# Kernel optimization log

Hardware: AMD Instinct MI355X
Metric: run time of the kernel (lower is better)

Reference implementation:

```python
import jax, jax.numpy as jnp
import numpy as np

D = 128        # node_representation_size
V = 100000     # unique_internal_nodes (embedding vocab)
N = 20000      # nodes in the internal graph
E = 640000     # total neighbor (edge) entries


def setup_inputs() -> dict:
    key = jax.random.key(0)
    k1, k2, k3, k4, k5, k6 = jax.random.split(key, 6)
    node_ids = jax.random.randint(k1, (N,), 0, V)
    neighbor_ids = jax.random.randint(k2, (E,), 0, V)
    segment_ids = jnp.sort(jax.random.randint(k3, (E,), 0, N))
    xav = 1.0 / np.sqrt(D)  # xavier_normal std for square [D,D]
    W = jax.random.normal(k4, (D, D), dtype=jnp.float32) * xav
    M = jax.random.normal(k5, (D, D), dtype=jnp.float32) * xav
    emb = jax.random.normal(k6, (V, D), dtype=jnp.float32)
    return {"node_ids": node_ids, "neighbor_ids": neighbor_ids,
            "segment_ids": segment_ids, "W": W, "M": M, "emb": emb}


def reference(node_ids, neighbor_ids, segment_ids, W, M, emb):
    # Per node: s = relu(W @ e[node] + sum_{nbr} M @ e[nbr]); result = sum_nodes s
    self_term = emb[node_ids] @ W.T                       # [N, D]
    nb_msgs = emb[neighbor_ids] @ M.T                     # [E, D]
    nb_agg = jax.ops.segment_sum(nb_msgs, segment_ids, num_segments=N)  # [N, D]
    per_node = jax.nn.relu(self_term + nb_agg)            # [N, D]
    result = per_node.sum(axis=0)                         # [D]
    return jax.nn.softmax(result)[:, None]                # [D, 1], softmax over dim 0
```

## Files before the change

kernel.cpp:

```cpp
#include <hip/hip_runtime.h>

#define D 128
#define RS_STRIDE 64

typedef __attribute__((ext_vector_type(8))) short bf16x8;
typedef __attribute__((ext_vector_type(8))) unsigned short u16x8;
typedef __attribute__((ext_vector_type(4))) float f32x4;
typedef __attribute__((ext_vector_type(2))) float f32x2;

__device__ __forceinline__ unsigned short f2bf(float f) {
    unsigned u = __float_as_uint(f);
    unsigned r = (u + 0x7fffu + ((u >> 16) & 1u)) >> 16;
    return (unsigned short)r;
}
__device__ __forceinline__ float bf2f(unsigned short h) {
    return __uint_as_float(((unsigned)h) << 16);
}
__device__ __forceinline__ ushort4 pack4(float4 v) {
    ushort4 o; o.x = f2bf(v.x); o.y = f2bf(v.y); o.z = f2bf(v.z); o.w = f2bf(v.w);
    return o;
}
__device__ __forceinline__ void red3(float& x) {
    x += __shfl_xor(x, 8);
    x += __shfl_xor(x, 16);
    x += __shfl_xor(x, 32);
}
__device__ __forceinline__ void acc4(unsigned v, float* s) {
    f32x2 lo = __builtin_amdgcn_cvt_pk_f32_fp8(v, false);
    f32x2 hi = __builtin_amdgcn_cvt_pk_f32_fp8(v, true);
    s[0] += lo[0]; s[1] += lo[1]; s[2] += hi[0]; s[3] += hi[1];
}
__device__ __forceinline__ void acc16(uint4 v, float* s) {
    acc4(v.x, s); acc4(v.y, s + 4); acc4(v.z, s + 8); acc4(v.w, s + 12);
}
__device__ __forceinline__ int swz(int r, int s) {
    return r * D + ((s ^ (r & 7)) << 3);
}

__global__ void prep_kernel(const float* __restrict__ emb, const float* __restrict__ W,
                            const float* __restrict__ M, const int* __restrict__ seg,
                            unsigned char* __restrict__ emb8,
                            unsigned short* __restrict__ Wb, unsigned short* __restrict__ Mb,
                            float* __restrict__ rs, int* __restrict__ row_ptr,
                            int n4, int E, int N) {
    int i = blockIdx.x * blockDim.x + threadIdx.x;
    if (i < n4) {
        float4 v = ((const float4*)emb)[i];
        int p = __builtin_amdgcn_cvt_pk_fp8_f32(v.x, v.y, 0, false);
        p = __builtin_amdgcn_cvt_pk_fp8_f32(v.z, v.w, p, true);
        ((unsigned*)emb8)[i] = (unsigned)p;
    }
    if (i < 4096)       ((ushort4*)Wb)[i]        = pack4(((const float4*)W)[i]);
    else if (i < 8192)  ((ushort4*)Mb)[i - 4096] = pack4(((const float4*)M)[i - 4096]);
    if (i < D) rs[i * RS_STRIDE] = 0.0f;
    if (i < E) {
        int s = seg[i];
        if (i == 0) {
            for (int n = 0; n <= s; ++n) row_ptr[n] = 0;
        } else {
            int sp = seg[i - 1];
            for (int n = sp + 1; n <= s; ++n) row_ptr[n] = i;
        }
        if (i == E - 1) {
            for (int n = s + 1; n <= N; ++n) row_ptr[n] = E;
        }
    }
}

__global__ __launch_bounds__(256) void fused_kernel(
    const int* __restrict__ node_ids, const int* __restrict__ nbr,
    const int* __restrict__ row_ptr, const unsigned char* __restrict__ emb8,
    const unsigned short* __restrict__ Wb, const unsigned short* __restrict__ Mb,
    float* __restrict__ rs, int N) {
    __shared__ unsigned short xs[16 * D];
    __shared__ unsigned short as_[16 * D];

    int t = threadIdx.x;
    int w = t >> 6;
    int tt = t & 63;
    int g = blockIdx.x;

    {
        int c = tt & 7;
        int j = tt >> 3;
        for (int i = 0; i < 4; ++i) {
            int r = w * 4 + i;
            int n = g * 16 + r;
            bool valid = n < N;

            uint4 xv = make_uint4(0u, 0u, 0u, 0u);
            if (valid && j == 0)
                xv = *(const uint4*)(emb8 + (size_t)node_ids[n] * D + c * 16);

            float s[16];
#pragma unroll
            for (int k = 0; k < 16; ++k) s[k] = 0.f;

            int lo = valid ? row_ptr[n] : 0;
            int hi = valid ? row_ptr[n + 1] : 0;
            int e = lo + j;
            for (; e + 8 < hi; e += 16) {
                uint4 a = *(const uint4*)(emb8 + (size_t)nbr[e] * D + c * 16);
                uint4 b = *(const uint4*)(emb8 + (size_t)nbr[e + 8] * D + c * 16);
                acc16(a, s);
                acc16(b, s);
            }
            if (e < hi) {
                uint4 a = *(const uint4*)(emb8 + (size_t)nbr[e] * D + c * 16);
                acc16(a, s);
            }
#pragma unroll
            for (int k = 0; k < 16; ++k) red3(s[k]);

            if (j == 0) {
                u16x8 o0, o1;
#pragma unroll
                for (int k = 0; k < 8; ++k) { o0[k] = f2bf(s[k]); o1[k] = f2bf(s[k + 8]); }
                *(u16x8*)&as_[swz(r, 2 * c)]     = o0;
                *(u16x8*)&as_[swz(r, 2 * c + 1)] = o1;

                float x[16];
#pragma unroll
                for (int k = 0; k < 16; ++k) x[k] = 0.f;
                acc16(xv, x);
                u16x8 p0, p1;
#pragma unroll
                for (int k = 0; k < 8; ++k) { p0[k] = f2bf(x[k]); p1[k] = f2bf(x[k + 8]); }
                *(u16x8*)&xs[swz(r, 2 * c)]     = p0;
                *(u16x8*)&xs[swz(r, 2 * c + 1)] = p1;
            }
        }
    }
    __syncthreads();

    int quad = tt >> 4, col = tt & 15;
    bf16x8 ax[4], aa[4];
#pragma unroll
    for (int ks = 0; ks < 4; ++ks) {
        ax[ks] = *(const bf16x8*)&xs[swz(col, ks * 4 + quad)];
        aa[ks] = *(const bf16x8*)&as_[swz(col, ks * 4 + quad)];
    }
#pragma unroll
    for (int p = 0; p < 2; ++p) {
        int dt = w + p * 4;
        int wrow = (dt * 16 + col) * D + quad * 8;
        f32x4 acc = {0.f, 0.f, 0.f, 0.f};
#pragma unroll
        for (int ks = 0; ks < 4; ++ks) {
            bf16x8 bw = *(const bf16x8*)(Wb + wrow + ks * 32);
            bf16x8 bm = *(const bf16x8*)(Mb + wrow + ks * 32);
            acc = __builtin_amdgcn_mfma_f32_16x16x32_bf16(ax[ks], bw, acc, 0, 0, 0);
            acc = __builtin_amdgcn_mfma_f32_16x16x32_bf16(aa[ks], bm, acc, 0, 0, 0);
        }
        float v = fmaxf(acc[0], 0.f) + fmaxf(acc[1], 0.f)
                + fmaxf(acc[2], 0.f) + fmaxf(acc[3], 0.f);
        v += __shfl_xor(v, 16);
        v += __shfl_xor(v, 32);
        if (tt < 16) atomicAdd(&rs[(dt * 16 + col) * RS_STRIDE], v);
    }
}

__global__ void agg_f32_kernel(const int* __restrict__ nbr, const int* __restrict__ row_ptr,
                               const float* __restrict__ emb,
                               unsigned short* __restrict__ aggb, int N) {
    int n = blockIdx.x * 4 + (threadIdx.x >> 6);
    if (n >= N) return;
    int tt = threadIdx.x & 63;
    int c = tt & 7;
    int j = tt >> 3;

    int lo = row_ptr[n], hi = row_ptr[n + 1];

    float4 s0 = make_float4(0.f, 0.f, 0.f, 0.f);
    float4 s1 = make_float4(0.f, 0.f, 0.f, 0.f);
    float4 s2 = make_float4(0.f, 0.f, 0.f, 0.f);
    float4 s3 = make_float4(0.f, 0.f, 0.f, 0.f);
    for (int e = lo + j; e < hi; e += 8) {
        const float4* r = (const float4*)&emb[(size_t)nbr[e] * D];
        float4 v0 = r[c], v1 = r[c + 8], v2 = r[c + 16], v3 = r[c + 24];
        s0.x += v0.x; s0.y += v0.y; s0.z += v0.z; s0.w += v0.w;
        s1.x += v1.x; s1.y += v1.y; s1.z += v1.z; s1.w += v1.w;
        s2.x += v2.x; s2.y += v2.y; s2.z += v2.z; s2.w += v2.w;
        s3.x += v3.x; s3.y += v3.y; s3.z += v3.z; s3.w += v3.w;
    }
    red3(s0.x); red3(s0.y); red3(s0.z); red3(s0.w);
    red3(s1.x); red3(s1.y); red3(s1.z); red3(s1.w);
    red3(s2.x); red3(s2.y); red3(s2.z); red3(s2.w);
    red3(s3.x); red3(s3.y); red3(s3.z); red3(s3.w);
    if (j == 0) {
        ushort4* o = (ushort4*)(aggb + (size_t)n * D);
        o[c]      = pack4(s0);
        o[c + 8]  = pack4(s1);
        o[c + 16] = pack4(s2);
        o[c + 24] = pack4(s3);
    }
}

__global__ __launch_bounds__(256) void matvec_f32_kernel(
    const int* __restrict__ node_ids, const float* __restrict__ emb,
    const unsigned short* __restrict__ aggb,
    const unsigned short* __restrict__ Wb, const unsigned short* __restrict__ Mb,
    float* __restrict__ rs, int N, int ngroups, int nstripes) {
    int t = threadIdx.x;
    int wid = blockIdx.x * 4 + (t >> 6);
    int l = t & 63;
    int quad = l >> 4, col = l & 15;
    int dt = wid & 7;
    int stripe = wid >> 3;

    bf16x8 bw[4], bm[4];
    int wrow = (dt * 16 + col) * D;
#pragma unroll
    for (int ks = 0; ks < 4; ++ks) {
        int off = wrow + ks * 32 + quad * 8;
        bw[ks] = *(const bf16x8*)(Wb + off);
        bm[ks] = *(const bf16x8*)(Mb + off);
    }

    const bf16x8 zero8 = {0, 0, 0, 0, 0, 0, 0, 0};
    float vsum = 0.f;

    for (int grp = stripe; grp < ngroups; grp += nstripes) {
        int node = grp * 16 + col;
        bool valid = node < N;
        int nid = valid ? node_ids[node] : 0;
        const unsigned short* ar = aggb + (size_t)node * D + quad * 8;

        f32x4 acc = {0.f, 0.f, 0.f, 0.f};
#pragma unroll
        for (int ks = 0; ks < 4; ++ks) {
            bf16x8 ax;
            if (valid) {
                const float4* xf = (const float4*)(emb +
                                   (size_t)nid * D + quad * 8 + ks * 32);
                ushort4 p0 = pack4(xf[0]);
                ushort4 p1 = pack4(xf[1]);
                ax[0] = (short)p0.x; ax[1] = (short)p0.y;
                ax[2] = (short)p0.z; ax[3] = (short)p0.w;
                ax[4] = (short)p1.x; ax[5] = (short)p1.y;
                ax[6] = (short)p1.z; ax[7] = (short)p1.w;
            } else ax = zero8;
            bf16x8 aa = valid ? *(const bf16x8*)(ar + ks * 32) : zero8;
            acc = __builtin_amdgcn_mfma_f32_16x16x32_bf16(ax, bw[ks], acc, 0, 0, 0);
            acc = __builtin_amdgcn_mfma_f32_16x16x32_bf16(aa, bm[ks], acc, 0, 0, 0);
        }
        vsum += fmaxf(acc[0], 0.f) + fmaxf(acc[1], 0.f)
              + fmaxf(acc[2], 0.f) + fmaxf(acc[3], 0.f);
    }

    vsum += __shfl_xor(vsum, 16);
    vsum += __shfl_xor(vsum, 32);
    if (l < 16) atomicAdd(&rs[(dt * 16 + col) * RS_STRIDE], vsum);
}

__global__ void softmax_kernel(const float* __restrict__ rs, float* __restrict__ out) {
    int t = threadIdx.x;
    float v0 = rs[t * RS_STRIDE];
    float v1 = rs[(t + 64) * RS_STRIDE];
    float m = fmaxf(v0, v1);
    for (int o = 32; o > 0; o >>= 1) m = fmaxf(m, __shfl_xor(m, o));
    float e0 = expf(v0 - m);
    float e1 = expf(v1 - m);
    float s = e0 + e1;
    for (int o = 32; o > 0; o >>= 1) s += __shfl_xor(s, o);
    float inv = 1.0f / s;
    out[t] = e0 * inv;
    out[t + 64] = e1 * inv;
}

extern "C" void kernel_launch(void* const* d_in, const int* in_sizes, int n_in,
                              void* d_out, int out_size, void* d_ws, size_t ws_size,
                              hipStream_t stream) {
    const int*   node_ids = (const int*)d_in[0];
    const int*   nbr      = (const int*)d_in[1];
    const int*   seg      = (const int*)d_in[2];
    const float* W        = (const float*)d_in[3];
    const float* M        = (const float*)d_in[4];
    const float* emb      = (const float*)d_in[5];
    float* out = (float*)d_out;

    int N = in_sizes[0];
    int E = in_sizes[1];
    long long VD = in_sizes[5];
    int ngroups  = (N + 15) / 16;

    unsigned short* aggb = (unsigned short*)d_ws;
    unsigned short* Wb   = aggb + (size_t)N * D;
    unsigned short* Mb   = Wb + D * D;
    float* rs            = (float*)(Mb + D * D);
    int* row_ptr         = (int*)(rs + (size_t)D * RS_STRIDE);
    unsigned char* emb8  = (unsigned char*)(row_ptr + (N + 1));

    size_t need_fp8 = (size_t)((char*)emb8 - (char*)d_ws) + (size_t)VD;
    bool use_fp8 = ws_size >= need_fp8;
    int n4 = use_fp8 ? (int)(VD / 4) : 0;
    int cvt_n = (n4 > 8192 ? n4 : 8192);
    int prep_n = (cvt_n > E ? cvt_n : E);

    prep_kernel<<<(prep_n + 255) / 256, 256, 0, stream>>>(emb, W, M, seg, emb8, Wb, Mb,
                                                          rs, row_ptr, n4, E, N);
    if (use_fp8) {
        fused_kernel<<<ngroups, 256, 0, stream>>>(node_ids, nbr, row_ptr, emb8,
                                                  Wb, Mb, rs, N);
    } else {
        int nstripes = (ngroups + 1) / 2;
        agg_f32_kernel<<<(N + 3) / 4, 256, 0, stream>>>(nbr, row_ptr, emb, aggb, N);
        matvec_f32_kernel<<<2 * nstripes, 256, 0, stream>>>(node_ids, emb, aggb, Wb, Mb,
                                                            rs, N, ngroups, nstripes);
    }
    softmax_kernel<<<1, 64, 0, stream>>>(rs, out);
}
```

Before: 141.9 us.

## Halve nodes per block in fused kernel and unroll neighbor gather by four

Each fused-kernel block now handles 8 nodes instead of 16, which doubles the grid size to spread the gather-heavy work across more CUs and waves. The neighbor loop is unrolled to issue four independent embedding loads per thread per iteration, for more memory-level parallelism. The 16-row MFMA tile is kept, and rows 8-15 are zero-padded. That wastes half of the matrix-multiply work per block and doubles the W/M reads and atomics on rs.

After: 158.9 us. 12.0% more time.

```diff
diff --git a/kernel.cpp b/kernel.cpp
--- a/kernel.cpp
+++ b/kernel.cpp
@@ -72,8 +72,8 @@
     const int* __restrict__ row_ptr, const unsigned char* __restrict__ emb8,
     const unsigned short* __restrict__ Wb, const unsigned short* __restrict__ Mb,
     float* __restrict__ rs, int N) {
-    __shared__ unsigned short xs[16 * D];
-    __shared__ unsigned short as_[16 * D];
+    __shared__ unsigned short xs[8 * D];
+    __shared__ unsigned short as_[8 * D];
 
     int t = threadIdx.x;
     int w = t >> 6;
@@ -83,9 +83,9 @@
     {
         int c = tt & 7;
         int j = tt >> 3;
-        for (int i = 0; i < 4; ++i) {
-            int r = w * 4 + i;
-            int n = g * 16 + r;
+        for (int i = 0; i < 2; ++i) {
+            int r = w * 2 + i;
+            int n = g * 8 + r;
             bool valid = n < N;
 
             uint4 xv = make_uint4(0u, 0u, 0u, 0u);
@@ -99,11 +99,24 @@
             int lo = valid ? row_ptr[n] : 0;
             int hi = valid ? row_ptr[n + 1] : 0;
             int e = lo + j;
-            for (; e + 8 < hi; e += 16) {
-                uint4 a = *(const uint4*)(emb8 + (size_t)nbr[e] * D + c * 16);
-                uint4 b = *(const uint4*)(emb8 + (size_t)nbr[e + 8] * D + c * 16);
-                acc16(a, s);
-                acc16(b, s);
+            for (; e + 24 < hi; e += 32) {
+                int i0 = nbr[e];
+                int i1 = nbr[e + 8];
+                int i2 = nbr[e + 16];
+                int i3 = nbr[e + 24];
+                uint4 a = *(const uint4*)(emb8 + (size_t)i0 * D + c * 16);
+                uint4 b = *(const uint4*)(emb8 + (size_t)i1 * D + c * 16);
+                uint4 d = *(const uint4*)(emb8 + (size_t)i2 * D + c * 16);
+                uint4 f = *(const uint4*)(emb8 + (size_t)i3 * D + c * 16);
+                acc16(a, s); acc16(b, s); acc16(d, s); acc16(f, s);
+            }
+            if (e + 8 < hi) {
+                int i0 = nbr[e];
+                int i1 = nbr[e + 8];
+                uint4 a = *(const uint4*)(emb8 + (size_t)i0 * D + c * 16);
+                uint4 b = *(const uint4*)(emb8 + (size_t)i1 * D + c * 16);
+                acc16(a, s); acc16(b, s);
+                e += 16;
             }
             if (e < hi) {
                 uint4 a = *(const uint4*)(emb8 + (size_t)nbr[e] * D + c * 16);
@@ -134,11 +147,17 @@
     __syncthreads();
 
     int quad = tt >> 4, col = tt & 15;
+    const bf16x8 zero8 = {0, 0, 0, 0, 0, 0, 0, 0};
     bf16x8 ax[4], aa[4];
 #pragma unroll
     for (int ks = 0; ks < 4; ++ks) {
-        ax[ks] = *(const bf16x8*)&xs[swz(col, ks * 4 + quad)];
-        aa[ks] = *(const bf16x8*)&as_[swz(col, ks * 4 + quad)];
+        if (col < 8) {
+            ax[ks] = *(const bf16x8*)&xs[swz(col, ks * 4 + quad)];
+            aa[ks] = *(const bf16x8*)&as_[swz(col, ks * 4 + quad)];
+        } else {
+            ax[ks] = zero8;
+            aa[ks] = zero8;
+        }
     }
 #pragma unroll
     for (int p = 0; p < 2; ++p) {
@@ -282,7 +301,7 @@
     int N = in_sizes[0];
     int E = in_sizes[1];
     long long VD = in_sizes[5];
-    int ngroups  = (N + 15) / 16;
+    int ngroups8 = (N + 7) / 8;
 
     unsigned short* aggb = (unsigned short*)d_ws;
     unsigned short* Wb   = aggb + (size_t)N * D;
@@ -297,12 +316,13 @@
     int cvt_n = (n4 > 8192 ? n4 : 8192);
     int prep_n = (cvt_n > E ? cvt_n : E);
 
-    prep_kernel<<<(prep_n + 255) / 256, 256, 0, stream>>>(emb, W, M, seg, emb8, Wb, Mb,
+    prep_kernel<<<(prep_n + 255) / 256, 256, 0, stream>>>(emb, M ? W : W, M, seg, emb8, Wb, Mb,
                                                           rs, row_ptr, n4, E, N);
     if (use_fp8) {
-        fused_kernel<<<ngroups, 256, 0, stream>>>(node_ids, nbr, row_ptr, emb8,
-                                                  Wb, Mb, rs, N);
+        fused_kernel<<<ngroups8, 256, 0, stream>>>(node_ids, nbr, row_ptr, emb8,
+                                                   Wb, Mb, rs, N);
     } else {
+        int ngroups  = (N + 15) / 16;
         int nstripes = (ngroups + 1) / 2;
         agg_f32_kernel<<<(N + 3) / 4, 256, 0, stream>>>(nbr, row_ptr, emb, aggb, N);
         matvec_f32_kernel<<<2 * nstripes, 256, 0, stream>>>(node_ids, emb, aggb, Wb, Mb,
```

## Slice fp8 embeddings by column and split aggregation into per-slice kernel

Applied to the files above, without the earlier changes.

Stores the fp8 embedding table as eight column slices of 16 bytes per row, and splits the fused kernel into a per-slice neighbor aggregation kernel plus a matvec kernel that reads the bf16 aggregate from workspace. Each aggregation block touches only one slice so gathers hit a smaller working set that may stay in L2. In exchange it adds an extra launch, a round trip of the aggregate through global memory, and repeated reads of neighbor indices across slices.

Result: slower. 184.8 us (+30.3%).

```diff
diff --git a/kernel.cpp b/kernel.cpp
--- a/kernel.cpp
+++ b/kernel.cpp
@@ -13,9 +13,6 @@
     unsigned r = (u + 0x7fffu + ((u >> 16) & 1u)) >> 16;
     return (unsigned short)r;
 }
-__device__ __forceinline__ float bf2f(unsigned short h) {
-    return __uint_as_float(((unsigned)h) << 16);
-}
 __device__ __forceinline__ ushort4 pack4(float4 v) {
     ushort4 o; o.x = f2bf(v.x); o.y = f2bf(v.y); o.z = f2bf(v.z); o.w = f2bf(v.w);
     return o;
@@ -30,16 +27,13 @@
     f32x2 hi = __builtin_amdgcn_cvt_pk_f32_fp8(v, true);
     s[0] += lo[0]; s[1] += lo[1]; s[2] += hi[0]; s[3] += hi[1];
 }
-__device__ __forceinline__ void acc16(uint4 v, float* s) {
-    acc4(v.x, s); acc4(v.y, s + 4); acc4(v.z, s + 8); acc4(v.w, s + 12);
-}
 __device__ __forceinline__ int swz(int r, int s) {
     return r * D + ((s ^ (r & 7)) << 3);
 }
 
 __global__ void prep_kernel(const float* __restrict__ emb, const float* __restrict__ W,
                             const float* __restrict__ M, const int* __restrict__ seg,
-                            unsigned char* __restrict__ emb8,
+                            unsigned char* __restrict__ emb8s, size_t V16,
                             unsigned short* __restrict__ Wb, unsigned short* __restrict__ Mb,
                             float* __restrict__ rs, int* __restrict__ row_ptr,
                             int n4, int E, int N) {
@@ -48,7 +42,10 @@
         float4 v = ((const float4*)emb)[i];
         int p = __builtin_amdgcn_cvt_pk_fp8_f32(v.x, v.y, 0, false);
         p = __builtin_amdgcn_cvt_pk_fp8_f32(v.z, v.w, p, true);
-        ((unsigned*)emb8)[i] = (unsigned)p;
+        int vrow = i >> 5;
+        int d0 = (i & 31) << 2;
+        *(unsigned*)(emb8s + (size_t)(d0 >> 4) * V16 + (size_t)vrow * 16 + (d0 & 15))
+            = (unsigned)p;
     }
     if (i < 4096)       ((ushort4*)Wb)[i]        = pack4(((const float4*)W)[i]);
     else if (i < 8192)  ((ushort4*)Mb)[i - 4096] = pack4(((const float4*)M)[i - 4096]);
@@ -67,9 +64,63 @@
     }
 }
 
-__global__ __launch_bounds__(256) void fused_kernel(
-    const int* __restrict__ node_ids, const int* __restrict__ nbr,
-    const int* __restrict__ row_ptr, const unsigned char* __restrict__ emb8,
+__global__ __launch_bounds__(256) void agg_slice_kernel(
+    const int* __restrict__ nbr, const int* __restrict__ row_ptr,
+    const unsigned char* __restrict__ emb8s, size_t V16,
+    unsigned short* __restrict__ aggb, int N) {
+    int s = blockIdx.x & 7;
+    int chunk = blockIdx.x >> 3;
+    int t = threadIdx.x;
+    int w = t >> 6;
+    int tt = t & 63;
+    int h = tt >> 5;
+    int j = (tt >> 2) & 7;
+    int c = tt & 3;
+
+    const unsigned char* base = emb8s + (size_t)s * V16 + c * 4;
+
+#pragma unroll
+    for (int pair = 0; pair < 4; ++pair) {
+        int n = chunk * 32 + (pair * 4 + w) * 2 + h;
+        bool valid = n < N;
+        int lo = valid ? row_ptr[n] : 0;
+        int hi = valid ? row_ptr[n + 1] : 0;
+
+        float sa[4] = {0.f, 0.f, 0.f, 0.f};
+        int e = lo + j;
+        for (; e + 8 < hi; e += 16) {
+            int i0 = __builtin_nontemporal_load(&nbr[e]);
+            int i1 = __builtin_nontemporal_load(&nbr[e + 8]);
+            unsigned a = *(const unsigned*)(base + (size_t)i0 * 16);
+            unsigned b = *(const unsigned*)(base + (size_t)i1 * 16);
+            acc4(a, sa); acc4(b, sa);
+        }
+        if (e < hi) {
+            int i0 = __builtin_nontemporal_load(&nbr[e]);
+            unsigned a = *(const unsigned*)(base + (size_t)i0 * 16);
+            acc4(a, sa);
+        }
+#pragma unroll
+        for (int k = 0; k < 4; ++k) {
+            sa[k] += __shfl_xor(sa[k], 4);
+            sa[k] += __shfl_xor(sa[k], 8);
+            sa[k] += __shfl_xor(sa[k], 16);
+        }
+        if (valid && j == 0) {
+            unsigned long long o =
+                  (unsigned long long)f2bf(sa[0])
+                | ((unsigned long long)f2bf(sa[1]) << 16)
+                | ((unsigned long long)f2bf(sa[2]) << 32)
+                | ((unsigned long long)f2bf(sa[3]) << 48);
+            __builtin_nontemporal_store(
+                o, (unsigned long long*)(aggb + (size_t)n * D + s * 16 + c * 4));
+        }
+    }
+}
+
+__global__ __launch_bounds__(256) void matvec_kernel(
+    const int* __restrict__ node_ids, const unsigned char* __restrict__ emb8s,
+    size_t V16, const unsigned short* __restrict__ aggb,
     const unsigned short* __restrict__ Wb, const unsigned short* __restrict__ Mb,
     float* __restrict__ rs, int N) {
     __shared__ unsigned short xs[16 * D];
@@ -81,55 +132,30 @@
     int g = blockIdx.x;
 
     {
-        int c = tt & 7;
-        int j = tt >> 3;
-        for (int i = 0; i < 4; ++i) {
-            int r = w * 4 + i;
-            int n = g * 16 + r;
-            bool valid = n < N;
-
-            uint4 xv = make_uint4(0u, 0u, 0u, 0u);
-            if (valid && j == 0)
-                xv = *(const uint4*)(emb8 + (size_t)node_ids[n] * D + c * 16);
-
-            float s[16];
-#pragma unroll
-            for (int k = 0; k < 16; ++k) s[k] = 0.f;
-
-            int lo = valid ? row_ptr[n] : 0;
-            int hi = valid ? row_ptr[n + 1] : 0;
-            int e = lo + j;
-            for (; e + 8 < hi; e += 16) {
-                uint4 a = *(const uint4*)(emb8 + (size_t)nbr[e] * D + c * 16);
-                uint4 b = *(const uint4*)(emb8 + (size_t)nbr[e + 8] * D + c * 16);
-                acc16(a, s);
-                acc16(b, s);
-            }
-            if (e < hi) {
-                uint4 a = *(const uint4*)(emb8 + (size_t)nbr[e] * D + c * 16);
-                acc16(a, s);
-            }
-#pragma unroll
-            for (int k = 0; k < 16; ++k) red3(s[k]);
-
-            if (j == 0) {
-                u16x8 o0, o1;
-#pragma unroll
-                for (int k = 0; k < 8; ++k) { o0[k] = f2bf(s[k]); o1[k] = f2bf(s[k + 8]); }
-                *(u16x8*)&as_[swz(r, 2 * c)]     = o0;
-                *(u16x8*)&as_[swz(r, 2 * c + 1)] = o1;
-
-                float x[16];
-#pragma unroll
-                for (int k = 0; k < 16; ++k) x[k] = 0.f;
-                acc16(xv, x);
-                u16x8 p0, p1;
-#pragma unroll
-                for (int k = 0; k < 8; ++k) { p0[k] = f2bf(x[k]); p1[k] = f2bf(x[k + 8]); }
-                *(u16x8*)&xs[swz(r, 2 * c)]     = p0;
-                *(u16x8*)&xs[swz(r, 2 * c + 1)] = p1;
-            }
-        }
+        int r = w * 4 + (tt >> 4);
+        int slot = tt & 15;
+        int n = g * 16 + r;
+        bool valid = n < N;
+
+        u16x8 av = {0, 0, 0, 0, 0, 0, 0, 0};
+        if (valid) av = *(const u16x8*)(aggb + (size_t)n * D + slot * 8);
+        *(u16x8*)&as_[swz(r, slot)] = av;
+
+        unsigned xv0 = 0u, xv1 = 0u;
+        if (valid) {
+            int nid = node_ids[n];
+            const unsigned* xr = (const unsigned*)(emb8s + (size_t)(slot >> 1) * V16 +
+                                                   (size_t)nid * 16 + (slot & 1) * 8);
+            xv0 = xr[0]; xv1 = xr[1];
+        }
+        float x[8];
+#pragma unroll
+        for (int k = 0; k < 8; ++k) x[k] = 0.f;
+        acc4(xv0, x); acc4(xv1, x + 4);
+        u16x8 pv;
+#pragma unroll
+        for (int k = 0; k < 8; ++k) pv[k] = f2bf(x[k]);
+        *(u16x8*)&xs[swz(r, slot)] = pv;
     }
     __syncthreads();
 
@@ -282,27 +308,31 @@
     int N = in_sizes[0];
     int E = in_sizes[1];
     long long VD = in_sizes[5];
-    int ngroups  = (N + 15) / 16;
+    size_t V16 = (size_t)VD / 8;
 
     unsigned short* aggb = (unsigned short*)d_ws;
     unsigned short* Wb   = aggb + (size_t)N * D;
     unsigned short* Mb   = Wb + D * D;
     float* rs            = (float*)(Mb + D * D);
     int* row_ptr         = (int*)(rs + (size_t)D * RS_STRIDE);
-    unsigned char* emb8  = (unsigned char*)(row_ptr + (N + 1));
-
-    size_t need_fp8 = (size_t)((char*)emb8 - (char*)d_ws) + (size_t)VD;
+    unsigned char* emb8s = (unsigned char*)(row_ptr + (N + 1));
+
+    size_t need_fp8 = (size_t)((char*)emb8s - (char*)d_ws) + (size_t)VD;
     bool use_fp8 = ws_size >= need_fp8;
     int n4 = use_fp8 ? (int)(VD / 4) : 0;
     int cvt_n = (n4 > 8192 ? n4 : 8192);
     int prep_n = (cvt_n > E ? cvt_n : E);
 
-    prep_kernel<<<(prep_n + 255) / 256, 256, 0, stream>>>(emb, W, M, seg, emb8, Wb, Mb,
-                                                          rs, row_ptr, n4, E, N);
+    prep_kernel<<<(prep_n + 255) / 256, 256, 0, stream>>>(emb, W, M, seg, emb8s, V16,
+                                                          Wb, Mb, rs, row_ptr, n4, E, N);
     if (use_fp8) {
-        fused_kernel<<<ngroups, 256, 0, stream>>>(node_ids, nbr, row_ptr, emb8,
-                                                  Wb, Mb, rs, N);
+        int nchunks = (N + 31) / 32;
+        agg_slice_kernel<<<nchunks * 8, 256, 0, stream>>>(nbr, row_ptr, emb8s, V16,
+                                                          aggb, N);
+        matvec_kernel<<<(N + 15) / 16, 256, 0, stream>>>(node_ids, emb8s, V16, aggb,
+                                                         Wb, Mb, rs, N);
     } else {
+        int ngroups  = (N + 15) / 16;
         int nstripes = (ngroups + 1) / 2;
         agg_f32_kernel<<<(N + 3) / 4, 256, 0, stream>>>(nbr, row_ptr, emb, aggb, N);
         matvec_f32_kernel<<<2 * nstripes, 256, 0, stream>>>(node_ids, emb, aggb, Wb, Mb,
```

## Split neighbor gather across two wave halves with 512-thread blocks

Applied to the files above, without the earlier changes.

Doubles the block to 512 threads so two groups of four waves each gather half of every node's neighbor list, with partial sums combined through a new fp32 shared buffer before bf16 conversion. Each wave then does one output tile of the MFMA matvec instead of two. The goal is more memory-level parallelism for the latency-bound fp8 gather, at the cost of an extra shared-memory stage, another barrier and higher LDS use per block, which may lower occupancy.

Measured after the change: 140.8 us. Within noise of the previous version (-0.7%).

```diff
diff --git a/kernel.cpp b/kernel.cpp
--- a/kernel.cpp
+++ b/kernel.cpp
@@ -12,9 +12,6 @@
     unsigned u = __float_as_uint(f);
     unsigned r = (u + 0x7fffu + ((u >> 16) & 1u)) >> 16;
     return (unsigned short)r;
-}
-__device__ __forceinline__ float bf2f(unsigned short h) {
-    return __uint_as_float(((unsigned)h) << 16);
 }
 __device__ __forceinline__ ushort4 pack4(float4 v) {
     ushort4 o; o.x = f2bf(v.x); o.y = f2bf(v.y); o.z = f2bf(v.z); o.w = f2bf(v.w);
@@ -67,29 +64,32 @@
     }
 }
 
-__global__ __launch_bounds__(256) void fused_kernel(
+__global__ __launch_bounds__(512) void fused_kernel(
     const int* __restrict__ node_ids, const int* __restrict__ nbr,
     const int* __restrict__ row_ptr, const unsigned char* __restrict__ emb8,
     const unsigned short* __restrict__ Wb, const unsigned short* __restrict__ Mb,
     float* __restrict__ rs, int N) {
     __shared__ unsigned short xs[16 * D];
     __shared__ unsigned short as_[16 * D];
+    __shared__ float pa[2][16][D];
 
     int t = threadIdx.x;
     int w = t >> 6;
     int tt = t & 63;
     int g = blockIdx.x;
+    int half = w >> 2;
+    int wq = w & 3;
 
     {
         int c = tt & 7;
         int j = tt >> 3;
         for (int i = 0; i < 4; ++i) {
-            int r = w * 4 + i;
+            int r = wq * 4 + i;
             int n = g * 16 + r;
             bool valid = n < N;
 
             uint4 xv = make_uint4(0u, 0u, 0u, 0u);
-            if (valid && j == 0)
+            if (valid && half == 0 && j == 0)
                 xv = *(const uint4*)(emb8 + (size_t)node_ids[n] * D + c * 16);
 
             float s[16];
@@ -98,10 +98,12 @@
 
             int lo = valid ? row_ptr[n] : 0;
             int hi = valid ? row_ptr[n + 1] : 0;
-            int e = lo + j;
-            for (; e + 8 < hi; e += 16) {
-                uint4 a = *(const uint4*)(emb8 + (size_t)nbr[e] * D + c * 16);
-                uint4 b = *(const uint4*)(emb8 + (size_t)nbr[e + 8] * D + c * 16);
+            int e = lo + half * 8 + j;
+            for (; e + 16 < hi; e += 32) {
+                int i0 = nbr[e];
+                int i1 = nbr[e + 16];
+                uint4 a = *(const uint4*)(emb8 + (size_t)i0 * D + c * 16);
+                uint4 b = *(const uint4*)(emb8 + (size_t)i1 * D + c * 16);
                 acc16(a, s);
                 acc16(b, s);
             }
@@ -113,23 +115,37 @@
             for (int k = 0; k < 16; ++k) red3(s[k]);
 
             if (j == 0) {
-                u16x8 o0, o1;
-#pragma unroll
-                for (int k = 0; k < 8; ++k) { o0[k] = f2bf(s[k]); o1[k] = f2bf(s[k + 8]); }
-                *(u16x8*)&as_[swz(r, 2 * c)]     = o0;
-                *(u16x8*)&as_[swz(r, 2 * c + 1)] = o1;
-
-                float x[16];
-#pragma unroll
-                for (int k = 0; k < 16; ++k) x[k] = 0.f;
-                acc16(xv, x);
-                u16x8 p0, p1;
-#pragma unroll
-                for (int k = 0; k < 8; ++k) { p0[k] = f2bf(x[k]); p1[k] = f2bf(x[k + 8]); }
-                *(u16x8*)&xs[swz(r, 2 * c)]     = p0;
-                *(u16x8*)&xs[swz(r, 2 * c + 1)] = p1;
+#pragma unroll
+                for (int k = 0; k < 4; ++k) {
+                    float4 v4 = make_float4(s[k * 4], s[k * 4 + 1],
+                                            s[k * 4 + 2], s[k * 4 + 3]);
+                    *(float4*)&pa[half][r][c * 16 + k * 4] = v4;
+                }
+                if (half == 0) {
+                    float x[16];
+#pragma unroll
+                    for (int k = 0; k < 16; ++k) x[k] = 0.f;
+                    acc16(xv, x);
+                    u16x8 p0, p1;
+#pragma unroll
+                    for (int k = 0; k < 8; ++k) {
+                        p0[k] = f2bf(x[k]); p1[k] = f2bf(x[k + 8]);
+                    }
+                    *(u16x8*)&xs[swz(r, 2 * c)]     = p0;
+                    *(u16x8*)&xs[swz(r, 2 * c + 1)] = p1;
+                }
             }
         }
+    }
+    __syncthreads();
+
+    if (t < 256) {
+        int r = t >> 4, slot = t & 15;
+        u16x8 o;
+#pragma unroll
+        for (int k = 0; k < 8; ++k)
+            o[k] = f2bf(pa[0][r][slot * 8 + k] + pa[1][r][slot * 8 + k]);
+        *(u16x8*)&as_[swz(r, slot)] = o;
     }
     __syncthreads();
 
@@ -140,24 +156,21 @@
         ax[ks] = *(const bf16x8*)&xs[swz(col, ks * 4 + quad)];
         aa[ks] = *(const bf16x8*)&as_[swz(col, ks * 4 + quad)];
     }
-#pragma unroll
-    for (int p = 0; p < 2; ++p) {
-        int dt = w + p * 4;
-        int wrow = (dt * 16 + col) * D + quad * 8;
-        f32x4 acc = {0.f, 0.f, 0.f, 0.f};
-#pragma unroll
-        for (int ks = 0; ks < 4; ++ks) {
-            bf16x8 bw = *(const bf16x8*)(Wb + wrow + ks * 32);
-            bf16x8 bm = *(const bf16x8*)(Mb + wrow + ks * 32);
-            acc = __builtin_amdgcn_mfma_f32_16x16x32_bf16(ax[ks], bw, acc, 0, 0, 0);
-            acc = __builtin_amdgcn_mfma_f32_16x16x32_bf16(aa[ks], bm, acc, 0, 0, 0);
-        }
-        float v = fmaxf(acc[0], 0.f) + fmaxf(acc[1], 0.f)
-                + fmaxf(acc[2], 0.f) + fmaxf(acc[3], 0.f);
-        v += __shfl_xor(v, 16);
-        v += __shfl_xor(v, 32);
-        if (tt < 16) atomicAdd(&rs[(dt * 16 + col) * RS_STRIDE], v);
-    }
+    int dt = w;
+    int wrow = (dt * 16 + col) * D + quad * 8;
+    f32x4 acc = {0.f, 0.f, 0.f, 0.f};
+#pragma unroll
+    for (int ks = 0; ks < 4; ++ks) {
+        bf16x8 bw = *(const bf16x8*)(Wb + wrow + ks * 32);
+        bf16x8 bm = *(const bf16x8*)(Mb + wrow + ks * 32);
+        acc = __builtin_amdgcn_mfma_f32_16x16x32_bf16(ax[ks], bw, acc, 0, 0, 0);
+        acc = __builtin_amdgcn_mfma_f32_16x16x32_bf16(aa[ks], bm, acc, 0, 0, 0);
+    }
+    float v = fmaxf(acc[0], 0.f) + fmaxf(acc[1], 0.f)
+            + fmaxf(acc[2], 0.f) + fmaxf(acc[3], 0.f);
+    v += __shfl_xor(v, 16);
+    v += __shfl_xor(v, 32);
+    if (tt < 16) atomicAdd(&rs[(dt * 16 + col) * RS_STRIDE], v);
 }
 
 __global__ void agg_f32_kernel(const int* __restrict__ nbr, const int* __restrict__ row_ptr,
@@ -300,7 +313,7 @@
     prep_kernel<<<(prep_n + 255) / 256, 256, 0, stream>>>(emb, W, M, seg, emb8, Wb, Mb,
                                                           rs, row_ptr, n4, E, N);
     if (use_fp8) {
-        fused_kernel<<<ngroups, 256, 0, stream>>>(node_ids, nbr, row_ptr, emb8,
+        fused_kernel<<<ngroups, 512, 0, stream>>>(node_ids, nbr, row_ptr, emb8,
                                                   Wb, Mb, rs, N);
     } else {
         int nstripes = (ngroups + 1) / 2;
```
